# Optimization experiments

Measured on AMD Instinct MI355X. Metric: run time of the kernel, lower is better.

Reference implementation:

```python
import jax, jax.numpy as jnp
import numpy as np

BLOCK_SIZE = 32
NUM_PROJS = 7


def _unit_hamming(n):
    # AngularLSH._unit_hamming_distance_array (Gray-code-like permutation)
    a = np.array([0, 1], dtype=np.int32)
    for i in range(1, n):
        a = np.concatenate([a, a[::-1] + 2 ** i])
    return a


def _lsh_hash(x, proj_dir, perm, enc_vec):
    # x: [B,H,N,D], proj_dir: [1,1,D,P] -> hash ids [B,H,N]
    pd = proj_dir[0, 0]  # [D,P]
    proj = jnp.einsum('bhnd,dp->bhnp', x, pd)
    bits = (proj > 0).astype(jnp.int32)
    bin_ids = (bits * enc_vec).sum(-1)
    return perm[bin_ids]


def _causal_attn(q, k, v):
    # q,k,v: [B,N,H,D] (xformers layout), causal softmax attention
    B, N, H, D = q.shape
    s = jnp.einsum('bqhd,bkhd->bhqk', q, k) * (D ** -0.5)
    causal = jnp.tril(jnp.ones((N, N), dtype=bool))
    s = jnp.where(causal, s, jnp.finfo(s.dtype).min)
    w = jax.nn.softmax(s, axis=-1)
    return jnp.einsum('bhqk,bkhd->bqhd', w, v)


def _forward(q, k, v, proj_dir):
    B, N, H, D = q.shape
    bs = BLOCK_SIZE
    nb = N // bs
    perm = jnp.asarray(_unit_hamming(NUM_PROJS))
    enc_vec = jnp.asarray(2 ** np.arange(NUM_PROJS, dtype=np.int32))

    qt = jnp.transpose(q, (0, 2, 1, 3))  # [B,H,N,D]
    kt = jnp.transpose(k, (0, 2, 1, 3))

    q_hash = _lsh_hash(qt, proj_dir, perm, enc_vec)  # [B,H,N]
    sort_idx = jnp.argsort(q_hash, axis=2, stable=True)
    q_hash_sort = jnp.take_along_axis(q_hash, sort_idx, axis=2)
    inv_idx = jnp.argsort(sort_idx, axis=2, stable=True)
    q_sorted = jnp.take_along_axis(qt, sort_idx[..., None], axis=2)  # [B,H,N,D]

    k_hash = _lsh_hash(kt, proj_dir, perm, enc_vec)  # [B,H,N]

    # torch .view(seq_len, -1) on [B,H,N] contiguous tensors (C-order reshape)
    qh_rows = q_hash_sort.reshape(N, -1)  # [N, B*H]
    kh_rows = k_hash.reshape(N, -1)
    eq = (qh_rows == kh_rows).reshape(nb, -1)  # rows grouped by query block
    keep = (eq.sum(axis=1) > 0)  # [nb] block kept if any hash match

    # K_split_per_block = k.reshape(B, nb, -1, D) on [B,H,N,D]
    k_blocks = kt.reshape(B, nb, (H * N) // nb, D)
    k_blocks = k_blocks * keep[None, :, None, None].astype(kt.dtype)
    k_crit = k_blocks.reshape(B, H, N, D)

    # out_critical = attn(q_critical, k_critical, v_critical) then unsort
    out = _causal_attn(jnp.transpose(q_sorted, (0, 2, 1, 3)),
                       jnp.transpose(k_crit, (0, 2, 1, 3)),
                       v)  # [B,N,H,D]
    out = jnp.take_along_axis(jnp.transpose(out, (0, 2, 1, 3)), inv_idx[..., None], axis=2)
    return jnp.transpose(out, (0, 2, 1, 3))  # [B,N,H,D]


def setup_inputs() -> dict:
    key = jax.random.key(0)
    k1, k2, k3, k4 = jax.random.split(key, 4)
    B, N, H, D = 2, 2048, 16, 128
    return {
        'q': jax.random.normal(k1, (B, N, H, D), dtype=jnp.float32),
        'k': jax.random.normal(k2, (B, N, H, D), dtype=jnp.float32),
        'v': jax.random.normal(k3, (B, N, H, D), dtype=jnp.float32),
        'proj_dir': jax.random.normal(k4, (1, 1, D, NUM_PROJS), dtype=jnp.float32),
        'is_causal': 1,
        'mask': jnp.zeros((1, 1), dtype=bool),
    }


def reference(q, k, v, proj_dir, is_causal, mask):
    # is_causal is always True at every attention call site; mask is unused then.
    return _forward(q, k, v, proj_dir)
```

## Files before the change

### kernel.cpp

```cpp
#include <hip/hip_runtime.h>
#include <cstdint>

#define BB 2
#define NN 2048
#define HH 16
#define DD 128
#define BH 32
#define NPROJ 7

typedef __bf16 bf16x8 __attribute__((ext_vector_type(8)));
typedef float f32x4 __attribute__((ext_vector_type(4)));

__device__ __forceinline__ unsigned short f2bf(float f) {
  unsigned int u = __float_as_uint(f);
  u += 0x7fff + ((u >> 16) & 1);
  return (unsigned short)(u >> 16);
}

__device__ __forceinline__ bf16x8 load_q8(const float* p) {
  float4 a = *(const float4*)p;
  float4 b = *(const float4*)(p + 4);
  unsigned short r[8] = {f2bf(a.x), f2bf(a.y), f2bf(a.z), f2bf(a.w),
                         f2bf(b.x), f2bf(b.y), f2bf(b.z), f2bf(b.w)};
  return *(bf16x8*)r;
}

__global__ void prep_kernel(const float* __restrict__ q, const float* __restrict__ k,
                            const float* __restrict__ v, const float* __restrict__ pd,
                            int* __restrict__ qh, int* __restrict__ kh,
                            unsigned short* __restrict__ Vt, unsigned short* __restrict__ Kb) {
  __shared__ __align__(16) char smem[64 * 132 * 2];
  if (blockIdx.x < 4096) {
    float* spd = (float*)smem;
    for (int i = threadIdx.x; i < DD * NPROJ; i += 256) spd[i] = pd[i];
    __syncthreads();
    long long gid = (long long)blockIdx.x * 256 + threadIdx.x;
    int part = (int)(gid & 7);
    long long row = gid >> 3;
    const long long NR = (long long)BB * NN * HH;
    int isk = row >= NR;
    long long r = isk ? row - NR : row;
    const float* src = (isk ? k : q) + r * DD + part * 16;
    double acc[NPROJ];
    for (int p = 0; p < NPROJ; ++p) acc[p] = 0.0;
    __align__(16) unsigned short kb16[16];
    for (int d = 0; d < 16; d += 4) {
      float4 x = *(const float4*)(src + d);
      if (isk) {
        kb16[d + 0] = f2bf(x.x); kb16[d + 1] = f2bf(x.y);
        kb16[d + 2] = f2bf(x.z); kb16[d + 3] = f2bf(x.w);
      }
      int dbase = part * 16 + d;
      for (int p = 0; p < NPROJ; ++p) {
        acc[p] += (double)x.x * (double)spd[(dbase + 0) * NPROJ + p]
                + (double)x.y * (double)spd[(dbase + 1) * NPROJ + p]
                + (double)x.z * (double)spd[(dbase + 2) * NPROJ + p]
                + (double)x.w * (double)spd[(dbase + 3) * NPROJ + p];
      }
    }
    int b_ = (int)(r / (NN * HH));
    int rem = (int)(r % (NN * HH));
    int n_ = rem / HH, h_ = rem % HH;
    if (isk) {
      unsigned short* dst = Kb + (((long long)(b_ * HH + h_) * NN + n_) << 7) + part * 16;
      *(uint4*)dst = *(const uint4*)&kb16[0];
      *(uint4*)(dst + 8) = *(const uint4*)&kb16[8];
    }
    for (int off = 1; off < 8; off <<= 1)
      for (int p = 0; p < NPROJ; ++p) acc[p] += __shfl_xor(acc[p], off);
    if (part == 0) {
      int bin = 0;
      for (int p = 0; p < NPROJ; ++p) bin |= ((int)(acc[p] > 0.0)) << p;
      int hsh = bin ^ (bin >> 1);
      (isk ? kh : qh)[((long long)b_ * HH + h_) * NN + n_] = hsh;
    }
  } else {
    unsigned short (*tile)[132] = (unsigned short(*)[132])smem;
    int blk = blockIdx.x - 4096;
    int bh = blk >> 5;
    int n0 = (blk & 31) * 64;
    int b = bh >> 4, h = bh & 15;
    for (int it = 0; it < 8; ++it) {
      int cid = it * 256 + threadIdx.x;
      int r = cid >> 5, d4 = (cid & 31) * 4;
      float4 x = *(const float4*)(v + (((long long)(b * NN + n0 + r) * HH + h) << 7) + d4);
      *(ushort4*)&tile[r][d4] = make_ushort4(f2bf(x.x), f2bf(x.y), f2bf(x.z), f2bf(x.w));
    }
    __syncthreads();
    for (int it = 0; it < 8; ++it) {
      int cid = it * 256 + threadIdx.x;
      int d = cid >> 4, n4 = (cid & 15) * 4;
      ushort4 y = make_ushort4(tile[n4 + 0][d], tile[n4 + 1][d], tile[n4 + 2][d], tile[n4 + 3][d]);
      *(ushort4*)(Vt + ((long long)bh * DD + d) * NN + n0 + n4) = y;
    }
  }
}

__global__ void sortkeep_kernel(const int* __restrict__ qh, const int* __restrict__ kh,
                                int* __restrict__ sidx, int* __restrict__ keep) {
  __shared__ int sh[NN];
  __shared__ int cnt[4][128];
  __shared__ int cum[128];
  __shared__ int kflag[2];
  int bh = blockIdx.x;
  const int* src = qh + (long long)bh * NN;
  for (int i = threadIdx.x; i < NN; i += 512) sh[i] = src[i];
  if (threadIdx.x < 2) kflag[threadIdx.x] = 0;
  __syncthreads();
  int bin = threadIdx.x & 127, seg = threadIdx.x >> 7;
  int n0 = seg * (NN / 4);
  int c = 0;
  for (int n = n0; n < n0 + NN / 4; ++n) c += (sh[n] == bin);
  cnt[seg][bin] = c;
  __syncthreads();
  if (threadIdx.x == 0) {
    int run = 0;
    for (int t = 0; t < 128; ++t) {
      cum[t] = run;
      run += cnt[0][t] + cnt[1][t] + cnt[2][t] + cnt[3][t];
    }
  }
  __syncthreads();
  int pos = cum[bin];
  for (int s = 0; s < seg; ++s) pos += cnt[s][bin];
  int f0 = 0, f1 = 0;
  for (int n = n0; n < n0 + NN / 4; ++n)
    if (sh[n] == bin) {
      sidx[(long long)bh * NN + pos] = n;
      int match = (bin == kh[(long long)bh * NN + pos]);
      if (pos < 1024) f0 |= match; else f1 |= match;
      ++pos;
    }
  if (f0) atomicOr(&kflag[0], 1);
  if (f1) atomicOr(&kflag[1], 1);
  __syncthreads();
  if (threadIdx.x < 2) keep[bh * 2 + threadIdx.x] = kflag[threadIdx.x];
}

__global__ __launch_bounds__(256, 3)
void flash_kernel(const float* __restrict__ q, const unsigned short* __restrict__ Kb,
                  const unsigned short* __restrict__ Vt, const int* __restrict__ sidx,
                  const int* __restrict__ keep, float* __restrict__ out) {
  __shared__ __align__(16) unsigned short Kt[64 * 136];
  __shared__ __align__(16) unsigned short Vs[128 * 72];
  __shared__ __align__(16) unsigned short Pb[4][16 * 72];

  int bh = blockIdx.x;
  int qt = 31 - (int)blockIdx.y;
  int b = bh >> 4, h = bh & 15;
  int tid = threadIdx.x;
  int w = tid >> 6, lane = tid & 63;
  int l16 = lane & 15, qd = lane >> 4;

  const unsigned short* Kh = Kb + (long long)bh * NN * DD;
  const unsigned short* Vb = Vt + (long long)bh * DD * NN;
  const float scale = 0.088388347648318447f;

  const int ksr = tid >> 4;
  const int ksc = (tid & 15) * 8;
  const int vsr = tid >> 3;
  const int vsc = (tid & 7) * 8;

  uint4 kreg[4], vreg[4];

#define STAGE_LOAD(K0, KP)                                                            \
  {                                                                                   \
    if (KP) {                                                                         \
      _Pragma("unroll")                                                               \
      for (int it = 0; it < 4; ++it)                                                  \
        kreg[it] = *(const uint4*)(Kh + (long long)((K0) + it * 16 + ksr) * DD + ksc);\
    } else {                                                                          \
      _Pragma("unroll")                                                               \
      for (int it = 0; it < 4; ++it) kreg[it] = make_uint4(0, 0, 0, 0);               \
    }                                                                                 \
    _Pragma("unroll")                                                                 \
    for (int it = 0; it < 4; ++it)                                                    \
      vreg[it] = *(const uint4*)(Vb + (long long)(it * 32 + vsr) * NN + (K0) + vsc);  \
  }

#define STAGE_WRITE()                                                                 \
  {                                                                                   \
    _Pragma("unroll")                                                                 \
    for (int it = 0; it < 4; ++it)                                                    \
      *(uint4*)&Kt[(it * 16 + ksr) * 136 + ksc] = kreg[it];                           \
    _Pragma("unroll")                                                                 \
    for (int it = 0; it < 4; ++it)                                                    \
      *(uint4*)&Vs[(it * 32 + vsr) * 72 + vsc] = vreg[it];                            \
  }

  int qrow = qt * 64 + w * 16 + l16;

  bf16x8 qf[4];
  {
    int nq = sidx[bh * NN + qrow];
    const float* p0 = q + (((long long)(b * NN + nq) * HH + h) << 7) + qd * 8;
#pragma unroll
    for (int c = 0; c < 4; ++c) qf[c] = load_q8(p0 + c * 32);
  }
  f32x4 o[8];
#pragma unroll
  for (int i = 0; i < 8; ++i) o[i] = (f32x4){0.f, 0.f, 0.f, 0.f};
  float m = -__builtin_inff(), l = 0.f;

  STAGE_LOAD(0, keep[h * 4]);
  STAGE_WRITE();
  __syncthreads();

  for (int kb = 0; kb <= qt; ++kb) {
    if (kb < qt) STAGE_LOAD((kb + 1) * 64, keep[h * 4 + ((kb + 1) >> 3)]);

    int k0 = kb * 64;

    float s[16];
    __builtin_amdgcn_s_setprio(1);
#pragma unroll
    for (int t = 0; t < 4; ++t) {
      f32x4 a1 = (f32x4){0.f, 0.f, 0.f, 0.f};
#pragma unroll
      for (int c = 0; c < 4; ++c) {
        bf16x8 kf = *(const bf16x8*)&Kt[(t * 16 + l16) * 136 + c * 32 + qd * 8];
        a1 = __builtin_amdgcn_mfma_f32_16x16x32_bf16(kf, qf[c], a1, 0, 0, 0);
      }
      if (kb == qt) {
#pragma unroll
        for (int r = 0; r < 4; ++r) {
          int keyg = k0 + t * 16 + qd * 4 + r;
          s[t * 4 + r] = (keyg > qrow) ? -__builtin_inff() : a1[r] * scale;
        }
      } else {
#pragma unroll
        for (int r = 0; r < 4; ++r) s[t * 4 + r] = a1[r] * scale;
      }
    }
    __builtin_amdgcn_s_setprio(0);

    {
      float x0 = fmaxf(fmaxf(s[0], s[1]), fmaxf(s[2], s[3]));
      float x1 = fmaxf(fmaxf(s[4], s[5]), fmaxf(s[6], s[7]));
      float x2 = fmaxf(fmaxf(s[8], s[9]), fmaxf(s[10], s[11]));
      float x3 = fmaxf(fmaxf(s[12], s[13]), fmaxf(s[14], s[15]));
      float mloc = fmaxf(fmaxf(x0, x1), fmaxf(x2, x3));
      mloc = fmaxf(mloc, __shfl_xor(mloc, 16));
      mloc = fmaxf(mloc, __shfl_xor(mloc, 32));
      if (__any(mloc > m)) {
        float mnew = fmaxf(m, mloc);
        float alpha = __expf(m - mnew);
        float aO[4];
#pragma unroll
        for (int r = 0; r < 4; ++r) aO[r] = __shfl(alpha, qd * 4 + r);
#pragma unroll
        for (int c8 = 0; c8 < 8; ++c8)
#pragma unroll
          for (int r = 0; r < 4; ++r) o[c8][r] *= aO[r];
        l *= alpha;
        m = mnew;
      }
      float psum = 0.f;
#pragma unroll
      for (int t = 0; t < 4; ++t) {
        float p0 = __expf(s[t * 4 + 0] - m);
        float p1 = __expf(s[t * 4 + 1] - m);
        float p2 = __expf(s[t * 4 + 2] - m);
        float p3 = __expf(s[t * 4 + 3] - m);
        psum += (p0 + p1) + (p2 + p3);
        *(ushort4*)&Pb[w][l16 * 72 + t * 16 + qd * 4] =
            make_ushort4(f2bf(p0), f2bf(p1), f2bf(p2), f2bf(p3));
      }
      psum += __shfl_xor(psum, 16);
      psum += __shfl_xor(psum, 32);
      l += psum;
    }

    __builtin_amdgcn_s_setprio(1);
#pragma unroll
    for (int g = 0; g < 2; ++g) {
      bf16x8 pf = *(const bf16x8*)&Pb[w][l16 * 72 + g * 32 + qd * 8];
#pragma unroll
      for (int c8 = 0; c8 < 8; ++c8) {
        bf16x8 vf = *(const bf16x8*)&Vs[(c8 * 16 + l16) * 72 + g * 32 + qd * 8];
        o[c8] = __builtin_amdgcn_mfma_f32_16x16x32_bf16(pf, vf, o[c8], 0, 0, 0);
      }
    }
    __builtin_amdgcn_s_setprio(0);

    if (kb < qt) {
      __syncthreads();
      STAGE_WRITE();
      __syncthreads();
    }
  }

  float lO[4];
  int nO[4];
#pragma unroll
  for (int r = 0; r < 4; ++r) {
    lO[r] = __shfl(l, qd * 4 + r);
    nO[r] = sidx[(long long)bh * NN + qt * 64 + w * 16 + qd * 4 + r];
  }
#pragma unroll
  for (int r = 0; r < 4; ++r) {
    float inv = 1.f / lO[r];
    float* ob = out + (((long long)(b * NN + nO[r]) * HH + h) << 7) + l16;
#pragma unroll
    for (int c8 = 0; c8 < 8; ++c8)
      ob[c8 * 16] = o[c8][r] * inv;
  }
#undef STAGE_LOAD
#undef STAGE_WRITE
}

extern "C" void kernel_launch(void* const* d_in, const int* in_sizes, int n_in,
                              void* d_out, int out_size, void* d_ws, size_t ws_size,
                              hipStream_t stream) {
  const float* q = (const float*)d_in[0];
  const float* k = (const float*)d_in[1];
  const float* v = (const float*)d_in[2];
  const float* pd = (const float*)d_in[3];
  float* out = (float*)d_out;
  char* ws = (char*)d_ws;
  int* qh   = (int*)(ws + 0);
  int* kh   = (int*)(ws + (1u << 18));
  int* sidx = (int*)(ws + (2u << 18));
  int* keep = (int*)(ws + 3u * (1u << 18));
  unsigned short* Vt = (unsigned short*)(ws + (2u << 20));
  unsigned short* Kb = (unsigned short*)(ws + (18u << 20));

  prep_kernel<<<5120, 256, 0, stream>>>(q, k, v, pd, qh, kh, Vt, Kb);
  sortkeep_kernel<<<32, 512, 0, stream>>>(qh, kh, sidx, keep);
  flash_kernel<<<dim3(32, 32), 256, 0, stream>>>(q, Kb, Vt, sidx, keep, out);
}
```

Baseline: 344.1 us.

## Keep P in registers via 16x16x16 MFMA, exp2 softmax, wider sort block

The flash kernel no longer stages the softmax probabilities through a per-wave LDS buffer. It packs them into bf16 registers with v_cvt_pk_bf16_f32 and feeds them directly to 16x16x16 bf16 MFMAs, whose accumulator layout matches the QK^T output. The scale is folded into an exp2 constant with an FMA, removing a multiply and the __expf conversion, and occupancy is raised to 4 blocks per SM. The sort/keep kernel uses 1024 threads in 8 segments to shorten its serial scan loops. The trade-off is twice as many MFMA instructions, each half the K depth, plus higher register pressure under the stricter launch bound.

After: 339.7 us. About the same (-1.3%).

```diff
diff --git a/kernel.cpp b/kernel.cpp
--- a/kernel.cpp
+++ b/kernel.cpp
@@ -10,6 +10,8 @@
 
 typedef __bf16 bf16x8 __attribute__((ext_vector_type(8)));
 typedef float f32x4 __attribute__((ext_vector_type(4)));
+typedef short short4v __attribute__((ext_vector_type(4)));
+typedef unsigned int uint2v __attribute__((ext_vector_type(2)));
 
 __device__ __forceinline__ unsigned short f2bf(float f) {
   unsigned int u = __float_as_uint(f);
@@ -23,6 +25,27 @@
   unsigned short r[8] = {f2bf(a.x), f2bf(a.y), f2bf(a.z), f2bf(a.w),
                          f2bf(b.x), f2bf(b.y), f2bf(b.z), f2bf(b.w)};
   return *(bf16x8*)r;
+}
+
+__device__ __forceinline__ unsigned cvt_pk_bf16(float lo, float hi) {
+  unsigned r;
+  asm("v_cvt_pk_bf16_f32 %0, %1, %2" : "=v"(r) : "v"(lo), "v"(hi));
+  return r;
+}
+
+#if __has_builtin(__builtin_amdgcn_exp2f)
+#define EXP2(x) __builtin_amdgcn_exp2f(x)
+#else
+#define EXP2(x) exp2f(x)
+#endif
+
+__device__ __forceinline__ f32x4 mfma16(short4v a, short4v b, f32x4 c) {
+#if __has_builtin(__builtin_amdgcn_mfma_f32_16x16x16bf16_1k)
+  return __builtin_amdgcn_mfma_f32_16x16x16bf16_1k(a, b, c, 0, 0, 0);
+#else
+  asm("v_mfma_f32_16x16x16_bf16 %0, %1, %2, %0" : "+v"(c) : "v"(a), "v"(b));
+  return c;
+#endif
 }
 
 __global__ void prep_kernel(const float* __restrict__ q, const float* __restrict__ k,
@@ -99,32 +122,33 @@
 __global__ void sortkeep_kernel(const int* __restrict__ qh, const int* __restrict__ kh,
                                 int* __restrict__ sidx, int* __restrict__ keep) {
   __shared__ int sh[NN];
-  __shared__ int cnt[4][128];
+  __shared__ int cnt[8][128];
   __shared__ int cum[128];
   __shared__ int kflag[2];
   int bh = blockIdx.x;
   const int* src = qh + (long long)bh * NN;
-  for (int i = threadIdx.x; i < NN; i += 512) sh[i] = src[i];
+  for (int i = threadIdx.x; i < NN; i += 1024) sh[i] = src[i];
   if (threadIdx.x < 2) kflag[threadIdx.x] = 0;
   __syncthreads();
   int bin = threadIdx.x & 127, seg = threadIdx.x >> 7;
-  int n0 = seg * (NN / 4);
+  int n0 = seg * (NN / 8);
   int c = 0;
-  for (int n = n0; n < n0 + NN / 4; ++n) c += (sh[n] == bin);
+  for (int n = n0; n < n0 + NN / 8; ++n) c += (sh[n] == bin);
   cnt[seg][bin] = c;
   __syncthreads();
   if (threadIdx.x == 0) {
     int run = 0;
     for (int t = 0; t < 128; ++t) {
       cum[t] = run;
-      run += cnt[0][t] + cnt[1][t] + cnt[2][t] + cnt[3][t];
+      run += cnt[0][t] + cnt[1][t] + cnt[2][t] + cnt[3][t]
+           + cnt[4][t] + cnt[5][t] + cnt[6][t] + cnt[7][t];
     }
   }
   __syncthreads();
   int pos = cum[bin];
   for (int s = 0; s < seg; ++s) pos += cnt[s][bin];
   int f0 = 0, f1 = 0;
-  for (int n = n0; n < n0 + NN / 4; ++n)
+  for (int n = n0; n < n0 + NN / 8; ++n)
     if (sh[n] == bin) {
       sidx[(long long)bh * NN + pos] = n;
       int match = (bin == kh[(long long)bh * NN + pos]);
@@ -137,13 +161,12 @@
   if (threadIdx.x < 2) keep[bh * 2 + threadIdx.x] = kflag[threadIdx.x];
 }
 
-__global__ __launch_bounds__(256, 3)
+__global__ __launch_bounds__(256, 4)
 void flash_kernel(const float* __restrict__ q, const unsigned short* __restrict__ Kb,
                   const unsigned short* __restrict__ Vt, const int* __restrict__ sidx,
                   const int* __restrict__ keep, float* __restrict__ out) {
   __shared__ __align__(16) unsigned short Kt[64 * 136];
   __shared__ __align__(16) unsigned short Vs[128 * 72];
-  __shared__ __align__(16) unsigned short Pb[4][16 * 72];
 
   int bh = blockIdx.x;
   int qt = 31 - (int)blockIdx.y;
@@ -151,10 +174,11 @@
   int tid = threadIdx.x;
   int w = tid >> 6, lane = tid & 63;
   int l16 = lane & 15, qd = lane >> 4;
+  (void)w;
 
   const unsigned short* Kh = Kb + (long long)bh * NN * DD;
   const unsigned short* Vb = Vt + (long long)bh * DD * NN;
-  const float scale = 0.088388347648318447f;
+  const float CEXP = 0.1275174316582815f;
 
   const int ksr = tid >> 4;
   const int ksc = (tid & 15) * 8;
@@ -225,15 +249,16 @@
 #pragma unroll
         for (int r = 0; r < 4; ++r) {
           int keyg = k0 + t * 16 + qd * 4 + r;
-          s[t * 4 + r] = (keyg > qrow) ? -__builtin_inff() : a1[r] * scale;
+          s[t * 4 + r] = (keyg > qrow) ? -__builtin_inff() : a1[r];
         }
       } else {
 #pragma unroll
-        for (int r = 0; r < 4; ++r) s[t * 4 + r] = a1[r] * scale;
+        for (int r = 0; r < 4; ++r) s[t * 4 + r] = a1[r];
       }
     }
     __builtin_amdgcn_s_setprio(0);
 
+    short4v pf[4];
     {
       float x0 = fmaxf(fmaxf(s[0], s[1]), fmaxf(s[2], s[3]));
       float x1 = fmaxf(fmaxf(s[4], s[5]), fmaxf(s[6], s[7]));
@@ -244,7 +269,7 @@
       mloc = fmaxf(mloc, __shfl_xor(mloc, 32));
       if (__any(mloc > m)) {
         float mnew = fmaxf(m, mloc);
-        float alpha = __expf(m - mnew);
+        float alpha = EXP2((m - mnew) * CEXP);
         float aO[4];
 #pragma unroll
         for (int r = 0; r < 4; ++r) aO[r] = __shfl(alpha, qd * 4 + r);
@@ -255,16 +280,17 @@
         l *= alpha;
         m = mnew;
       }
+      float mc = m * CEXP;
       float psum = 0.f;
 #pragma unroll
       for (int t = 0; t < 4; ++t) {
-        float p0 = __expf(s[t * 4 + 0] - m);
-        float p1 = __expf(s[t * 4 + 1] - m);
-        float p2 = __expf(s[t * 4 + 2] - m);
-        float p3 = __expf(s[t * 4 + 3] - m);
+        float p0 = EXP2(__builtin_fmaf(s[t * 4 + 0], CEXP, -mc));
+        float p1 = EXP2(__builtin_fmaf(s[t * 4 + 1], CEXP, -mc));
+        float p2 = EXP2(__builtin_fmaf(s[t * 4 + 2], CEXP, -mc));
+        float p3 = EXP2(__builtin_fmaf(s[t * 4 + 3], CEXP, -mc));
         psum += (p0 + p1) + (p2 + p3);
-        *(ushort4*)&Pb[w][l16 * 72 + t * 16 + qd * 4] =
-            make_ushort4(f2bf(p0), f2bf(p1), f2bf(p2), f2bf(p3));
+        uint2v pk = {cvt_pk_bf16(p0, p1), cvt_pk_bf16(p2, p3)};
+        pf[t] = __builtin_bit_cast(short4v, pk);
       }
       psum += __shfl_xor(psum, 16);
       psum += __shfl_xor(psum, 32);
@@ -273,12 +299,11 @@
 
     __builtin_amdgcn_s_setprio(1);
 #pragma unroll
-    for (int g = 0; g < 2; ++g) {
-      bf16x8 pf = *(const bf16x8*)&Pb[w][l16 * 72 + g * 32 + qd * 8];
+    for (int t = 0; t < 4; ++t) {
 #pragma unroll
       for (int c8 = 0; c8 < 8; ++c8) {
-        bf16x8 vf = *(const bf16x8*)&Vs[(c8 * 16 + l16) * 72 + g * 32 + qd * 8];
-        o[c8] = __builtin_amdgcn_mfma_f32_16x16x32_bf16(pf, vf, o[c8], 0, 0, 0);
+        short4v vf = *(const short4v*)&Vs[(c8 * 16 + l16) * 72 + t * 16 + qd * 4];
+        o[c8] = mfma16(pf[t], vf, o[c8]);
       }
     }
     __builtin_amdgcn_s_setprio(0);
@@ -326,6 +351,6 @@
   unsigned short* Kb = (unsigned short*)(ws + (18u << 20));
 
   prep_kernel<<<5120, 256, 0, stream>>>(q, k, v, pd, qh, kh, Vt, Kb);
-  sortkeep_kernel<<<32, 512, 0, stream>>>(qh, kh, sidx, keep);
+  sortkeep_kernel<<<32, 1024, 0, stream>>>(qh, kh, sidx, keep);
   flash_kernel<<<dim3(32, 32), 256, 0, stream>>>(q, Kb, Vt, sidx, keep, out);
 }
```
